# Optimization experiments

Hardware: AMD Instinct MI355X
Metric: run time of the kernel (lower is better)

## Reference

```python
import math
import jax, jax.numpy as jnp
import numpy as np

NUM_DIRECTIONS = 10
NUM_PROMO_DIRECTIONS = 10
NUM_DROP_TYPES = 7
POLICY_SIZE = 81 * (NUM_DIRECTIONS + NUM_PROMO_DIRECTIONS + NUM_DROP_TYPES)  # 2187
DIRECTION_VECTORS = [(0, -1), (-1, -1), (1, -1), (-1, 0), (1, 0), (0, 1), (-1, 1), (1, 1), (-1, -2), (1, -2)]
SLIDING_DIRS = {0, 1, 2, 3, 4, 5, 6, 7}


def _move_to_direction(from_sq, to_sq):
    from_f, from_r = from_sq // 9, from_sq % 9
    to_f, to_r = to_sq // 9, to_sq % 9
    df, dr = to_f - from_f, to_r - from_r
    for idx, (vf, vr) in enumerate(DIRECTION_VECTORS):
        if idx in SLIDING_DIRS:
            if vf == 0 and vr == 0:
                continue
            if vf == 0:
                if df == 0 and dr != 0 and ((dr > 0) == (vr > 0)) and (dr % vr == 0):
                    return idx
            elif vr == 0:
                if dr == 0 and df != 0 and ((df > 0) == (vf > 0)) and (df % vf == 0):
                    return idx
            elif df != 0 and dr != 0 and (df % vf == 0) and (dr % vr == 0):
                dist_f, dist_r = df // vf, dr // vr
                if dist_f == dist_r and dist_f > 0:
                    return idx
        elif df == vf and dr == vr:
            return idx
    return -1


def _index_tables():
    from_to_dir = np.full(81 * 81, -1, dtype=np.int64)
    promo_elig = np.zeros(81 * 81, dtype=bool)
    for f in range(81):
        for t in range(81):
            d_idx = _move_to_direction(f, t)
            if d_idx >= 0:
                from_to_dir[f * 81 + t] = d_idx
                if (f % 9) <= 2 or (t % 9) <= 2:
                    promo_elig[f * 81 + t] = True
    valid = from_to_dir >= 0
    valid_idx = np.where(valid)[0]
    to_sqs = valid_idx % 81
    policy_idx = from_to_dir[valid_idx] * 81 + to_sqs
    promo_mask = valid & promo_elig
    promo_idx = np.where(promo_mask)[0]
    promo_policy_idx = (from_to_dir[promo_idx] + NUM_DIRECTIONS) * 81 + (promo_idx % 81)
    return (valid_idx.astype(np.int32), policy_idx.astype(np.int32),
            promo_idx.astype(np.int32), promo_policy_idx.astype(np.int32))


def setup_inputs() -> dict:
    key = jax.random.key(0)
    ks = jax.random.split(key, 8)
    B, D = 4096, 256
    s = 1.0 / math.sqrt(D)
    x = jax.random.normal(ks[0], (B, 81, D), dtype=jnp.float32)
    W_embed = jax.random.normal(ks[1], (D, D), dtype=jnp.float32) * s
    b_embed = jnp.zeros((D,), dtype=jnp.float32)
    Wq = jax.random.normal(ks[2], (D, D), dtype=jnp.float32) * s
    bq = jnp.zeros((D,), dtype=jnp.float32)
    Wk = jax.random.normal(ks[3], (D, D), dtype=jnp.float32) * s
    bk = jnp.zeros((D,), dtype=jnp.float32)
    drop_queries = jax.random.normal(ks[4], (NUM_DROP_TYPES, D), dtype=jnp.float32) * 0.02
    vi, pi, qi, qpi = _index_tables()
    return {"x": x, "W_embed": W_embed, "b_embed": b_embed, "Wq": Wq, "bq": bq,
            "Wk": Wk, "bk": bk, "drop_queries": drop_queries,
            "valid_idx": jnp.asarray(vi), "policy_idx": jnp.asarray(pi),
            "promo_idx": jnp.asarray(qi), "promo_policy_idx": jnp.asarray(qpi)}


def _mish(v):
    return v * jnp.tanh(jax.nn.softplus(v))


def reference(x, W_embed, b_embed, Wq, bq, Wk, bk, drop_queries,
              valid_idx, policy_idx, promo_idx, promo_policy_idx):
    B = x.shape[0]
    d = W_embed.shape[1]
    scale = 1.0 / math.sqrt(d)
    pe = _mish(x @ W_embed + b_embed)          # (B, 81, d)
    Q = pe @ Wq + bq                            # (B, 81, d)
    K = pe @ Wk + bk                            # (B, 81, d)
    board = jnp.einsum('bsd,btd->bst', Q, K) * scale   # (B, 81, 81)
    board_flat = board.reshape(B, 81 * 81)
    NEG = jnp.asarray(-1e10, dtype=x.dtype)
    policy = jnp.full((B, POLICY_SIZE), NEG, dtype=x.dtype)
    # board moves: scatter-amax of valid (from,to) logits into (dir, to) slots
    logit_values = board_flat[:, valid_idx]
    policy = policy.at[:, policy_idx].max(logit_values)
    # promotion moves: same logits, promo-eligible subset, shifted by 10 dirs
    promo_values = board_flat[:, promo_idx]
    policy = policy.at[:, promo_policy_idx].max(promo_values)
    # drops: learned queries vs K
    drop_logits = jnp.einsum('qd,btd->bqt', drop_queries, K) * scale  # (B, 7, 81)
    drop_start = (NUM_DIRECTIONS + NUM_PROMO_DIRECTIONS) * 81
    policy = policy.at[:, drop_start:drop_start + NUM_DROP_TYPES * 81].set(
        drop_logits.reshape(B, -1))
    return policy
```

## Files before the change

kernel.cpp:

```cpp
#include <hip/hip_runtime.h>

typedef unsigned short u16;
typedef unsigned int u32;
typedef unsigned char u8t;
using bfrag = __attribute__((ext_vector_type(8))) short;
using facc  = __attribute__((ext_vector_type(4))) float;

__device__ __forceinline__ u16 f2b(float f) {
  u32 u = __float_as_uint(f);
  return (u16)((u + 0x7FFFu + ((u >> 16) & 1u)) >> 16);
}
__device__ __forceinline__ float b2f(u16 h) { return __uint_as_float(((u32)h) << 16); }
__device__ __forceinline__ u32 encf(float f) {
  u32 u = __float_as_uint(f);
  return (u & 0x80000000u) ? ~u : (u | 0x80000000u);
}
__device__ __forceinline__ float decf(u32 e) {
  return __uint_as_float((e & 0x80000000u) ? (e & 0x7FFFFFFFu) : ~e);
}
__device__ __forceinline__ float mish_f(float v) {
  float ev = __expf(v);
  float d = __builtin_fmaf(ev, ev + 2.f, 2.f);
  return __builtin_fmaf(-2.f * v, __builtin_amdgcn_rcpf(d), v);
}
__device__ __forceinline__ float ldf(const void* p, int i, int bf) {
  return bf ? b2f(((const u16*)p)[i]) : ((const float*)p)[i];
}
__device__ __forceinline__ u8t f2fp8(float f) {
  return (u8t)(__builtin_amdgcn_cvt_pk_fp8_f32(f, f, 0, 0) & 0xFF);
}
__device__ __forceinline__ u32 pk4fp8(float a, float b, float c, float d) {
  u32 v = __builtin_amdgcn_cvt_pk_fp8_f32(a, b, 0, 0);
  return __builtin_amdgcn_cvt_pk_fp8_f32(c, d, v, 1);
}
__device__ __forceinline__ char* tp8(char* base, int row, int colb) {
  return base + ((row << 8) + (colb ^ ((row & 7) << 4)));
}

__global__ void detect_dtype_kernel(const void* __restrict__ x, int* __restrict__ flag) {
  __shared__ int cnt;
  const int tid = threadIdx.x;
  if (tid == 0) cnt = 0;
  __syncthreads();
  const u16* p = (const u16*)x;
  u16 h = p[tid * 96 + 4];
  int e = (int)((h >> 7) & 0xFF);
  if (e >= 116 && e <= 134) atomicAdd(&cnt, 1);
  __syncthreads();
  if (tid == 0) *flag = (cnt >= 128) ? 1 : 0;
}

__global__ void prep_all(const void* __restrict__ W_embed,
                         const void* __restrict__ Wq, const void* __restrict__ Wk,
                         const void* __restrict__ bq, const void* __restrict__ bk,
                         const void* __restrict__ dq,
                         const int* __restrict__ vi, const int* __restrict__ pi,
                         const int* __restrict__ qi, const int* __restrict__ qpi,
                         int nv, int np,
                         u8t* __restrict__ Wt8, u8t* __restrict__ Wqk8,
                         u8t* __restrict__ dqkp8, u8t* __restrict__ uvw_tl,
                         float* __restrict__ dqc,
                         u32* __restrict__ invP, const int* __restrict__ dflag) {
  __shared__ float wkrow[256];
  __shared__ u16 wqt[64][260];
  __shared__ u8t u8l[256], w8l[256];
  const int bid = blockIdx.x;
  const int bf = *dflag;
  const int t = threadIdx.x;

  if (bid < 256) {
    const int k = bid, n = t;
    u8t v = f2fp8(ldf(W_embed, (k << 8) + n, bf));
    int nt = n >> 4, lr = n & 15, kt = k >> 5, lg = (k >> 3) & 3, e = k & 7;
    Wt8[(((nt << 3) + kt) << 9) + (((lg << 4) + lr) << 3) + e] = v;
  } else if (bid < 512) {
    const int n = bid - 256, k = t;
    wkrow[k] = ldf(Wk, (n << 8) + k, bf);
    float s = 0.f;
    for (int d0 = 0; d0 < 256; d0 += 64) {
      __syncthreads();
      if (bf) {
        for (int sI = t; sI < 2048; sI += 256) {
          int kk = sI >> 3, dg = (sI & 7) << 3;
          bfrag v = *(const bfrag*)((const u16*)Wq + (kk << 8) + d0 + dg);
          #pragma unroll
          for (int e = 0; e < 8; ++e) wqt[dg + e][kk] = (u16)v[e];
        }
      } else {
        for (int sI = t; sI < 2048; sI += 256) {
          int kk = sI >> 3, dg = (sI & 7) << 3;
          const float* wp = (const float*)Wq + (kk << 8) + d0 + dg;
          float4 p0 = *(const float4*)wp, p1 = *(const float4*)(wp + 4);
          wqt[dg + 0][kk] = f2b(p0.x); wqt[dg + 1][kk] = f2b(p0.y);
          wqt[dg + 2][kk] = f2b(p0.z); wqt[dg + 3][kk] = f2b(p0.w);
          wqt[dg + 4][kk] = f2b(p1.x); wqt[dg + 5][kk] = f2b(p1.y);
          wqt[dg + 6][kk] = f2b(p1.z); wqt[dg + 7][kk] = f2b(p1.w);
        }
      }
      __syncthreads();
      #pragma unroll 8
      for (int dd = 0; dd < 64; ++dd) s += b2f(wqt[dd][k]) * wkrow[d0 + dd];
    }
    int nt = n >> 4, lr = n & 15, kt = k >> 5, lg = (k >> 3) & 3, e = k & 7;
    Wqk8[(((nt << 3) + kt) << 9) + (((lg << 4) + lr) << 3) + e] = f2fp8(s);
  } else if (bid < 519) {
    const int blk = bid - 512, d = t;
    float s = 0.f;
    for (int nn = 0; nn < 256; ++nn)
      s += ldf(Wk, (d << 8) + nn, bf) * ldf(dq, (blk << 8) + nn, bf);
    dqkp8[(blk << 8) + d] = f2fp8(s);
  } else if (bid == 519) {
    if (t < 7) {
      float s = 0.f;
      for (int nn = 0; nn < 256; ++nn) s += ldf(dq, (t << 8) + nn, bf) * ldf(bk, nn, bf);
      dqc[t] = s;
    } else if (t == 7) {
      float s = 0.f;
      for (int nn = 0; nn < 256; ++nn) s += ldf(bq, nn, bf) * ldf(bk, nn, bf);
      dqc[7] = s;
    }
  } else if (bid == 521) {
    for (int i = t; i < 6561; i += 256) invP[i] = 0u;
    __syncthreads();
    for (int i = t; i < nv; i += 256) atomicOr(&invP[vi[i]], (u32)(pi[i] + 1));
    for (int i = t; i < np; i += 256) atomicOr(&invP[qi[i]], ((u32)(qpi[i] + 1)) << 16);
  } else if (bid == 522) {
    {
      float su = 0.f, sw = 0.f;
      for (int nn = 0; nn < 256; ++nn) {
        su += ldf(Wq, (t << 8) + nn, bf) * ldf(bk, nn, bf);
        sw += ldf(Wk, (t << 8) + nn, bf) * ldf(bq, nn, bf);
      }
      u8l[t] = f2fp8(su);
      w8l[t] = f2fp8(sw);
    }
    __syncthreads();
    for (int s = t; s < 512; s += 256) {
      int kt = s >> 6, ln = s & 63, lr2 = ln & 15, lg2 = ln >> 4;
      #pragma unroll
      for (int e = 0; e < 8; ++e) {
        int k = kt * 32 + lg2 * 8 + e;
        u8t v = (lr2 == 0) ? u8l[k] : (lr2 == 1) ? w8l[k] : (u8t)0;
        uvw_tl[(s << 3) + e] = v;
      }
    }
  }
}

#define LDS_TOTAL 52864

__global__ __launch_bounds__(256, 3)
void dirpolicy_fp8(const void* __restrict__ x,
                   const void* __restrict__ b_embed,
                   const u8t* __restrict__ Wt8,
                   const u8t* __restrict__ Wqk8,
                   const u8t* __restrict__ dqkp8,
                   const u8t* __restrict__ uvw_tl,
                   const float* __restrict__ dqc,
                   const u32* __restrict__ invP,
                   void* __restrict__ out,
                   const int* __restrict__ dflag) {
  extern __shared__ char smem[];
  char* bufA = smem;
  char* bufP = smem + 22528;
  u32* pol = (u32*)(smem + 43264);
  float* alpha = (float*)(smem + 52012);
  float* beta  = (float*)(smem + 52396);
  float* dqcS  = (float*)(smem + 52780);

  const int tid = threadIdx.x;
  const int lane = tid & 63;
  const int w = tid >> 6;
  const int lr = lane & 15;
  const int lg = lane >> 4;
  const int isbf = *dflag;
  const int b = blockIdx.x;
  const u32 ENEG = encf(-1e10f);

  for (int i = tid; i < 1792; i += 256) {
    int q = i >> 8, d = i & 255;
    *tp8(bufA, 81 + q, d) = dqkp8[i];
  }
  for (int i = tid; i < 2187; i += 256) pol[i] = ENEG;
  if (tid < 8) dqcS[tid] = dqc[tid];

  if (isbf) {
    const u16* xb = (const u16*)x + (size_t)b * 20736u;
    #pragma unroll 2
    for (int c = 0; c < 11; ++c) {
      int idx = tid + (c << 8);
      if (idx < 2592) {
        bfrag v = *(const bfrag*)(xb + (idx << 3));
        u32 lo = pk4fp8(b2f((u16)v[0]), b2f((u16)v[1]), b2f((u16)v[2]), b2f((u16)v[3]));
        u32 hi = pk4fp8(b2f((u16)v[4]), b2f((u16)v[5]), b2f((u16)v[6]), b2f((u16)v[7]));
        uint2 pk; pk.x = lo; pk.y = hi;
        *(uint2*)tp8(bufA, idx >> 5, (idx & 31) << 3) = pk;
      }
    }
  } else {
    const float4* xs = (const float4*)((const float*)x + (size_t)b * 20736u);
    #pragma unroll 2
    for (int c = 0; c < 11; ++c) {
      int idx = tid + (c << 8);
      if (idx < 2592) {
        float4 p0 = xs[idx * 2], p1 = xs[idx * 2 + 1];
        u32 lo = pk4fp8(p0.x, p0.y, p0.z, p0.w);
        u32 hi = pk4fp8(p1.x, p1.y, p1.z, p1.w);
        uint2 pk; pk.x = lo; pk.y = hi;
        *(uint2*)tp8(bufA, idx >> 5, (idx & 31) << 3) = pk;
      }
    }
  }
  __syncthreads();

  #pragma unroll 1
  for (int rh = 0; rh < 2; ++rh) {
    #pragma unroll 1
    for (int jh = 0; jh < 2; ++jh) {
      facc acc[3][2];
      facc z4 = {0.f, 0.f, 0.f, 0.f};
      #pragma unroll
      for (int i = 0; i < 3; ++i)
        #pragma unroll
        for (int jj = 0; jj < 2; ++jj) acc[i][jj] = z4;
      #pragma unroll
      for (int kt = 0; kt < 8; ++kt) {
        long bb[2], a[3];
        #pragma unroll
        for (int jj = 0; jj < 2; ++jj)
          bb[jj] = *(const long*)(Wt8 + (((((w << 2) + (jh << 1) + jj) << 3) + kt) << 9) + (lane << 3));
        #pragma unroll
        for (int i = 0; i < 3; ++i)
          a[i] = *(const long*)tp8(bufA, rh * 48 + i * 16 + lr, (kt << 5) + (lg << 3));
        #pragma unroll
        for (int i = 0; i < 3; ++i)
          #pragma unroll
          for (int jj = 0; jj < 2; ++jj)
            acc[i][jj] = __builtin_amdgcn_mfma_f32_16x16x32_fp8_fp8(bb[jj], a[i], acc[i][jj], 0, 0, 0);
      }
      #pragma unroll
      for (int jj = 0; jj < 2; ++jj) {
        const int dbase = (w << 6) + ((jh << 1) + jj) * 16 + (lg << 2);
        const float b0 = ldf(b_embed, dbase + 0, isbf);
        const float b1 = ldf(b_embed, dbase + 1, isbf);
        const float b2 = ldf(b_embed, dbase + 2, isbf);
        const float b3 = ldf(b_embed, dbase + 3, isbf);
        #pragma unroll
        for (int i = 0; i < 3; ++i) {
          const int row = rh * 48 + i * 16 + lr;
          if (row < 81) {
            u32 pk4 = pk4fp8(mish_f(acc[i][jj][0] + b0), mish_f(acc[i][jj][1] + b1),
                             mish_f(acc[i][jj][2] + b2), mish_f(acc[i][jj][3] + b3));
            *(u32*)tp8(bufP, row, dbase) = pk4;
          }
        }
      }
    }
  }
  __syncthreads();

  if (w < 3) {
    facc ae0, ae1;
    {
      facc z4 = {0.f, 0.f, 0.f, 0.f};
      ae0 = z4; ae1 = z4;
    }
    #pragma unroll
    for (int kt = 0; kt < 8; ++kt) {
      long av = *(const long*)(uvw_tl + (kt << 9) + (lane << 3));
      long b0 = *(const long*)tp8(bufP, (w << 5) + lr, (kt << 5) + (lg << 3));
      long b1 = *(const long*)tp8(bufP, (w << 5) + 16 + lr, (kt << 5) + (lg << 3));
      ae0 = __builtin_amdgcn_mfma_f32_16x16x32_fp8_fp8(av, b0, ae0, 0, 0, 0);
      ae1 = __builtin_amdgcn_mfma_f32_16x16x32_fp8_fp8(av, b1, ae1, 0, 0, 0);
    }
    if (lg == 0) {
      const float c7 = dqcS[7];
      const int col0 = (w << 5) + lr, col1 = col0 + 16;
      if (col0 < 81) { alpha[col0] = (ae0[0] + c7) * 0.0625f; beta[col0] = ae0[1] * 0.0625f; }
      if (col1 < 81) { alpha[col1] = (ae1[0] + c7) * 0.0625f; beta[col1] = ae1[1] * 0.0625f; }
    }
  }

  #pragma unroll 1
  for (int rh = 0; rh < 2; ++rh) {
    #pragma unroll 1
    for (int jh = 0; jh < 2; ++jh) {
      facc acc2[3][2];
      facc z4 = {0.f, 0.f, 0.f, 0.f};
      #pragma unroll
      for (int i = 0; i < 3; ++i)
        #pragma unroll
        for (int jj = 0; jj < 2; ++jj) acc2[i][jj] = z4;
      #pragma unroll
      for (int kt = 0; kt < 8; ++kt) {
        long bb[2], a[3];
        #pragma unroll
        for (int jj = 0; jj < 2; ++jj)
          bb[jj] = *(const long*)(Wqk8 + (((((w << 2) + (jh << 1) + jj) << 3) + kt) << 9) + (lane << 3));
        #pragma unroll
        for (int i = 0; i < 3; ++i)
          a[i] = *(const long*)tp8(bufP, rh * 48 + i * 16 + lr, (kt << 5) + (lg << 3));
        #pragma unroll
        for (int i = 0; i < 3; ++i)
          #pragma unroll
          for (int jj = 0; jj < 2; ++jj)
            acc2[i][jj] = __builtin_amdgcn_mfma_f32_16x16x32_fp8_fp8(bb[jj], a[i], acc2[i][jj], 0, 0, 0);
      }
      #pragma unroll
      for (int jj = 0; jj < 2; ++jj) {
        const int dbase = (w << 6) + ((jh << 1) + jj) * 16 + (lg << 2);
        #pragma unroll
        for (int i = 0; i < 3; ++i) {
          const int row = rh * 48 + i * 16 + lr;
          if (row < 81) {
            u32 pk4 = pk4fp8(acc2[i][jj][0], acc2[i][jj][1], acc2[i][jj][2], acc2[i][jj][3]);
            *(u32*)tp8(bufA, row, dbase) = pk4;
          }
        }
      }
    }
  }
  __syncthreads();

  const int wr4 = w >> 1;
  const int wc4 = w & 1;
  #pragma unroll 1
  for (int pass = 0; pass < 2; ++pass) {
    const int nj = pass ? 1 : 2;
    const int jb = pass ? 2 : 0;
    facc bd[3][2];
    {
      facc z4 = {0.f, 0.f, 0.f, 0.f};
      #pragma unroll
      for (int i = 0; i < 3; ++i)
        #pragma unroll
        for (int jj = 0; jj < 2; ++jj) bd[i][jj] = z4;
    }
    #pragma unroll
    for (int kt = 0; kt < 8; ++kt) {
      long a[3], bb[2];
      #pragma unroll
      for (int i = 0; i < 3; ++i)
        a[i] = *(const long*)tp8(bufA, wr4 * 48 + i * 16 + lr, (kt << 5) + (lg << 3));
      #pragma unroll
      for (int jj = 0; jj < 2; ++jj)
        bb[jj] = (jj < nj)
          ? *(const long*)tp8(bufP, wc4 * 48 + (jb + jj) * 16 + lr, (kt << 5) + (lg << 3))
          : 0L;
      #pragma unroll
      for (int i = 0; i < 3; ++i)
        #pragma unroll
        for (int jj = 0; jj < 2; ++jj)
          if (jj < nj)
            bd[i][jj] = __builtin_amdgcn_mfma_f32_16x16x32_fp8_fp8(a[i], bb[jj], bd[i][jj], 0, 0, 0);
    }
    #pragma unroll
    for (int jj = 0; jj < 2; ++jj) {
      if (jj >= nj) continue;
      const int colb = wc4 * 48 + (jb + jj) * 16 + lr;
      const float betv = (colb < 81) ? beta[colb] : 0.f;
      #pragma unroll
      for (int i = 0; i < 3; ++i)
        #pragma unroll
        for (int r = 0; r < 4; ++r) {
          const int rowb = wr4 * 48 + i * 16 + (lg << 2) + r;
          if (rowb < 81) {
            if (colb < 81) {
              const u32 ev = encf(bd[i][jj][r] * 0.0625f + alpha[rowb] + betv);
              const u32 pv = invP[rowb * 81 + colb];
              if (pv & 0xFFFFu) atomicMax(&pol[(pv & 0xFFFFu) - 1], ev);
              if (pv >> 16)     atomicMax(&pol[(pv >> 16) - 1], ev);
            }
          } else if (rowb < 88 && colb < 81) {
            pol[1620 + (rowb - 81) * 81 + colb] =
                encf((bd[i][jj][r] + dqcS[rowb - 81]) * 0.0625f);
          }
        }
    }
  }
  __syncthreads();

  if (isbf) {
    u16* ob = (u16*)out + (size_t)b * 2187u;
    for (int p2 = tid; p2 < 2187; p2 += 256) ob[p2] = f2b(decf(pol[p2]));
  } else {
    float* ob = (float*)out + (size_t)b * 2187u;
    for (int p2 = tid; p2 < 2187; p2 += 256) ob[p2] = decf(pol[p2]);
  }
}

extern "C" void kernel_launch(void* const* d_in, const int* in_sizes, int n_in,
                              void* d_out, int out_size, void* d_ws, size_t ws_size,
                              hipStream_t stream) {
  const void* x        = d_in[0];
  const void* W_embed  = d_in[1];
  const void* b_embed  = d_in[2];
  const void* Wq       = d_in[3];
  const void* bq       = d_in[4];
  const void* Wk       = d_in[5];
  const void* bk_      = d_in[6];
  const void* dq       = d_in[7];
  const int* valid_idx         = (const int*)d_in[8];
  const int* policy_idx        = (const int*)d_in[9];
  const int* promo_idx         = (const int*)d_in[10];
  const int* promo_policy_idx  = (const int*)d_in[11];
  const int n_valid = in_sizes[8];
  const int n_promo = in_sizes[10];
  const int B = in_sizes[0] / 20736;

  char* ws = (char*)d_ws;
  u8t* Wt8     = (u8t*)(ws);
  u8t* Wqk8    = (u8t*)(ws + 65536);
  u8t* dqkp8   = (u8t*)(ws + 131072);
  u8t* uvw_tl  = (u8t*)(ws + 133120);
  float* dqc   = (float*)(ws + 137216);
  int* dflag   = (int*)(ws + 137248);
  u32* invP    = (u32*)(ws + 137280);
  if (ws_size < 164000) return;

  detect_dtype_kernel<<<dim3(1), dim3(256), 0, stream>>>(x, dflag);
  prep_all<<<dim3(523), dim3(256), 0, stream>>>(
      W_embed, Wq, Wk, bq, bk_, dq,
      valid_idx, policy_idx, promo_idx, promo_policy_idx, n_valid, n_promo,
      Wt8, Wqk8, dqkp8, uvw_tl, dqc, invP, dflag);

  (void)hipFuncSetAttribute((const void*)dirpolicy_fp8,
                            hipFuncAttributeMaxDynamicSharedMemorySize, LDS_TOTAL);
  if (B > 0)
    dirpolicy_fp8<<<dim3(B), dim3(256), LDS_TOTAL, stream>>>(
        x, b_embed, Wt8, Wqk8, dqkp8, uvw_tl, dqc, invP, d_out, dflag);
}
```

Measured before the change: 285.0 us.

## Load x directly from global as bf16 in embed GEMM, drop LDS fp8 staging

Removes the up-front conversion of the input block to fp8 in LDS and instead loads x fragments straight from global memory inside the MFMA loop, converting to bf16. The embedding weights are prepacked as bf16 and the embed GEMM switches from fp8 to bf16 MFMA, improving precision. This removes a staging pass and a barrier but makes each wave re-read x from global/cache repeatedly across jh passes and waves, with per-element conversion in the inner loop.

```diff
diff --git a/kernel.cpp b/kernel.cpp
--- a/kernel.cpp
+++ b/kernel.cpp
@@ -35,6 +35,20 @@
 }
 __device__ __forceinline__ char* tp8(char* base, int row, int colb) {
   return base + ((row << 8) + (colb ^ ((row & 7) << 4)));
+}
+__device__ __forceinline__ bfrag load_xfrag(const void* x, long idx, int isbf) {
+  if (isbf) {
+    return *(const bfrag*)((const u16*)x + idx);
+  } else {
+    const float* xf = (const float*)x + idx;
+    float4 p0 = *(const float4*)xf, p1 = *(const float4*)(xf + 4);
+    bfrag o;
+    o[0] = (short)f2b(p0.x); o[1] = (short)f2b(p0.y);
+    o[2] = (short)f2b(p0.z); o[3] = (short)f2b(p0.w);
+    o[4] = (short)f2b(p1.x); o[5] = (short)f2b(p1.y);
+    o[6] = (short)f2b(p1.z); o[7] = (short)f2b(p1.w);
+    return o;
+  }
 }
 
 __global__ void detect_dtype_kernel(const void* __restrict__ x, int* __restrict__ flag) {
@@ -57,7 +71,7 @@
                          const int* __restrict__ vi, const int* __restrict__ pi,
                          const int* __restrict__ qi, const int* __restrict__ qpi,
                          int nv, int np,
-                         u8t* __restrict__ Wt8, u8t* __restrict__ Wqk8,
+                         u16* __restrict__ Wt16, u8t* __restrict__ Wqk8,
                          u8t* __restrict__ dqkp8, u8t* __restrict__ uvw_tl,
                          float* __restrict__ dqc,
                          u32* __restrict__ invP, const int* __restrict__ dflag) {
@@ -70,9 +84,10 @@
 
   if (bid < 256) {
     const int k = bid, n = t;
-    u8t v = f2fp8(ldf(W_embed, (k << 8) + n, bf));
+    u16 v = bf ? ((const u16*)W_embed)[(k << 8) + n]
+               : f2b(((const float*)W_embed)[(k << 8) + n]);
     int nt = n >> 4, lr = n & 15, kt = k >> 5, lg = (k >> 3) & 3, e = k & 7;
-    Wt8[(((nt << 3) + kt) << 9) + (((lg << 4) + lr) << 3) + e] = v;
+    Wt16[(((nt << 3) + kt) << 9) + (((lg << 4) + lr) << 3) + e] = v;
   } else if (bid < 512) {
     const int n = bid - 256, k = t;
     wkrow[k] = ldf(Wk, (n << 8) + k, bf);
@@ -152,7 +167,7 @@
 __global__ __launch_bounds__(256, 3)
 void dirpolicy_fp8(const void* __restrict__ x,
                    const void* __restrict__ b_embed,
-                   const u8t* __restrict__ Wt8,
+                   const u16* __restrict__ Wt16,
                    const u8t* __restrict__ Wqk8,
                    const u8t* __restrict__ dqkp8,
                    const u8t* __restrict__ uvw_tl,
@@ -184,35 +199,7 @@
   for (int i = tid; i < 2187; i += 256) pol[i] = ENEG;
   if (tid < 8) dqcS[tid] = dqc[tid];
 
-  if (isbf) {
-    const u16* xb = (const u16*)x + (size_t)b * 20736u;
-    #pragma unroll 2
-    for (int c = 0; c < 11; ++c) {
-      int idx = tid + (c << 8);
-      if (idx < 2592) {
-        bfrag v = *(const bfrag*)(xb + (idx << 3));
-        u32 lo = pk4fp8(b2f((u16)v[0]), b2f((u16)v[1]), b2f((u16)v[2]), b2f((u16)v[3]));
-        u32 hi = pk4fp8(b2f((u16)v[4]), b2f((u16)v[5]), b2f((u16)v[6]), b2f((u16)v[7]));
-        uint2 pk; pk.x = lo; pk.y = hi;
-        *(uint2*)tp8(bufA, idx >> 5, (idx & 31) << 3) = pk;
-      }
-    }
-  } else {
-    const float4* xs = (const float4*)((const float*)x + (size_t)b * 20736u);
-    #pragma unroll 2
-    for (int c = 0; c < 11; ++c) {
-      int idx = tid + (c << 8);
-      if (idx < 2592) {
-        float4 p0 = xs[idx * 2], p1 = xs[idx * 2 + 1];
-        u32 lo = pk4fp8(p0.x, p0.y, p0.z, p0.w);
-        u32 hi = pk4fp8(p1.x, p1.y, p1.z, p1.w);
-        uint2 pk; pk.x = lo; pk.y = hi;
-        *(uint2*)tp8(bufA, idx >> 5, (idx & 31) << 3) = pk;
-      }
-    }
-  }
-  __syncthreads();
-
+  const long xbase = (long)b * 20736;
   #pragma unroll 1
   for (int rh = 0; rh < 2; ++rh) {
     #pragma unroll 1
@@ -225,18 +212,21 @@
         for (int jj = 0; jj < 2; ++jj) acc[i][jj] = z4;
       #pragma unroll
       for (int kt = 0; kt < 8; ++kt) {
-        long bb[2], a[3];
+        bfrag bb[2], a[3];
         #pragma unroll
         for (int jj = 0; jj < 2; ++jj)
-          bb[jj] = *(const long*)(Wt8 + (((((w << 2) + (jh << 1) + jj) << 3) + kt) << 9) + (lane << 3));
-        #pragma unroll
-        for (int i = 0; i < 3; ++i)
-          a[i] = *(const long*)tp8(bufA, rh * 48 + i * 16 + lr, (kt << 5) + (lg << 3));
+          bb[jj] = *(const bfrag*)(Wt16 + (((((w << 2) + (jh << 1) + jj) << 3) + kt) << 9) + (lane << 3));
+        #pragma unroll
+        for (int i = 0; i < 3; ++i) {
+          int row = rh * 48 + i * 16 + lr;
+          if (row > 80) row = 80;
+          a[i] = load_xfrag(x, xbase + (long)row * 256 + (kt << 5) + (lg << 3), isbf);
+        }
         #pragma unroll
         for (int i = 0; i < 3; ++i)
           #pragma unroll
           for (int jj = 0; jj < 2; ++jj)
-            acc[i][jj] = __builtin_amdgcn_mfma_f32_16x16x32_fp8_fp8(bb[jj], a[i], acc[i][jj], 0, 0, 0);
+            acc[i][jj] = __builtin_amdgcn_mfma_f32_16x16x32_bf16(bb[jj], a[i], acc[i][jj], 0, 0, 0);
       }
       #pragma unroll
       for (int jj = 0; jj < 2; ++jj) {
@@ -409,24 +399,24 @@
   const int B = in_sizes[0] / 20736;
 
   char* ws = (char*)d_ws;
-  u8t* Wt8     = (u8t*)(ws);
-  u8t* Wqk8    = (u8t*)(ws + 65536);
-  u8t* dqkp8   = (u8t*)(ws + 131072);
-  u8t* uvw_tl  = (u8t*)(ws + 133120);
-  float* dqc   = (float*)(ws + 137216);
-  int* dflag   = (int*)(ws + 137248);
-  u32* invP    = (u32*)(ws + 137280);
-  if (ws_size < 164000) return;
+  u16* Wt16    = (u16*)(ws);
+  u8t* Wqk8    = (u8t*)(ws + 131072);
+  u8t* dqkp8   = (u8t*)(ws + 196608);
+  u8t* uvw_tl  = (u8t*)(ws + 198656);
+  float* dqc   = (float*)(ws + 202752);
+  int* dflag   = (int*)(ws + 202784);
+  u32* invP    = (u32*)(ws + 202816);
+  if (ws_size < 230000) return;
 
   detect_dtype_kernel<<<dim3(1), dim3(256), 0, stream>>>(x, dflag);
   prep_all<<<dim3(523), dim3(256), 0, stream>>>(
       W_embed, Wq, Wk, bq, bk_, dq,
       valid_idx, policy_idx, promo_idx, promo_policy_idx, n_valid, n_promo,
-      Wt8, Wqk8, dqkp8, uvw_tl, dqc, invP, dflag);
+      Wt16, Wqk8, dqkp8, uvw_tl, dqc, invP, dflag);
 
   (void)hipFuncSetAttribute((const void*)dirpolicy_fp8,
                             hipFuncAttributeMaxDynamicSharedMemorySize, LDS_TOTAL);
   if (B > 0)
     dirpolicy_fp8<<<dim3(B), dim3(256), LDS_TOTAL, stream>>>(
-        x, b_embed, Wt8, Wqk8, dqkp8, uvw_tl, dqc, invP, d_out, dflag);
-}
+        x, b_embed, Wt16, Wqk8, dqkp8, uvw_tl, dqc, invP, d_out, dflag);
+}
```

After: 565.7 us. +98.5%, slower.
